# Kernel tuning notes

Hardware: AMD Instinct MI355X
Metric: run time of the kernel (lower is better)

## Reference

```python
import jax, jax.numpy as jnp
import numpy as np

B, N, D = 4, 4096, 512
K = 16384          # codebook size
NUM_Q = 2          # residual quantizers (shared codebook)


def setup_inputs() -> dict:
    key = jax.random.key(0)
    ks = jax.random.split(key, 6)
    s = 1.0 / np.sqrt(D)
    return {
        "x": jax.random.normal(ks[0], (B, N, D), dtype=jnp.float32),
        "enc_w": jax.random.normal(ks[1], (D, D), dtype=jnp.float32) * s,
        "enc_b": jnp.zeros((D,), dtype=jnp.float32),
        "codebook": jax.random.normal(ks[2], (K, D), dtype=jnp.float32),
        "dec_w": jax.random.normal(ks[3], (D, D), dtype=jnp.float32) * s,
        "dec_b": jnp.zeros((D,), dtype=jnp.float32),
    }


def _residual_vq(z, codebook):
    # z: [B, N, D] -> flatten tokens
    flat = z.reshape(-1, z.shape[-1])          # [T, D]
    c_sq = jnp.sum(codebook * codebook, axis=-1)  # [K]
    q_sum = jnp.zeros_like(flat)
    residual = flat
    for _ in range(NUM_Q):
        # argmin of ||r - c||^2 == argmin of (||c||^2 - 2 r.c); skip ||r||^2
        dists = c_sq[None, :] - 2.0 * (residual @ codebook.T)  # [T, K]
        idx = jnp.argmin(dists, axis=-1)                       # [T]
        q = codebook[idx]                                      # gather [T, D]
        q_sum = q_sum + q
        residual = residual - q
    return q_sum.reshape(z.shape)


def reference(x, enc_w, enc_b, codebook, dec_w, dec_b):
    z = x @ enc_w.T + enc_b                     # encoder Linear(512 -> 512)
    q = _residual_vq(z, codebook)               # sum of per-stage code vectors
    z_tilde = z + jax.lax.stop_gradient(q - z)  # straight-through estimator
    x_recon = z_tilde @ dec_w.T + dec_b         # decoder Linear(512 -> 512)
    return x_recon
```

## Files before the change

kernel.cpp:

```cpp
#include <hip/hip_runtime.h>
#include <stdint.h>

constexpr int TT = 16384;
constexpr int DD = 512;
constexpr int KK = 16384;
constexpr int TOPK = 8;

typedef __bf16 bf16x8 __attribute__((ext_vector_type(8)));
typedef __bf16 bf16x4 __attribute__((ext_vector_type(4)));
typedef float f32x4 __attribute__((ext_vector_type(4)));

typedef const __attribute__((address_space(1))) void* gas_ptr;
typedef __attribute__((address_space(3))) void* las_ptr;

__device__ __forceinline__ unsigned long long pack_di(float d, int idx) {
    uint32_t u = __float_as_uint(d);
    u = (u & 0x80000000u) ? ~u : (u | 0x80000000u);
    return ((unsigned long long)u << 32) | (uint32_t)idx;
}

__device__ __forceinline__ unsigned long long umin64(unsigned long long a,
                                                     unsigned long long b) {
    return a < b ? a : b;
}
__device__ __forceinline__ uint32_t umin32(uint32_t a, uint32_t b) { return a < b ? a : b; }
__device__ __forceinline__ uint32_t umax32(uint32_t a, uint32_t b) { return a > b ? a : b; }

__device__ __forceinline__ uint32_t sortable(float d) {
    uint32_t u = __float_as_uint(d);
    return u ^ ((uint32_t)((int32_t)u >> 31) | 0x80000000u);
}

template<int MODE>
__global__ __launch_bounds__(256)
void gemm_mfma(const float* __restrict__ A, const float* __restrict__ A2,
               const float* __restrict__ W, const float* __restrict__ bias,
               float* __restrict__ out0, float* __restrict__ out1,
               __bf16* __restrict__ out2)
{
    __shared__ __bf16 Ah[128 * 64], Al[128 * 64];
    __shared__ __bf16 Bh[128 * 64], Bl[128 * 64];
    const int tid = threadIdx.x;
    const int lane = tid & 63;
    const int w = tid >> 6;
    const int row0 = blockIdx.y * 128;
    const int col0 = blockIdx.x * 128;

    f32x4 acc[2][8] = {};

    const int sr = tid >> 4;
    const int scol = (tid & 15) * 4;
    const int lcol = (((scol >> 3) ^ (sr & 7)) << 3) + (scol & 7);

    int a_off[2], b_off[8];
    #pragma unroll
    for (int mi = 0; mi < 2; ++mi) {
        const int ar = w * 32 + mi * 16 + (lane & 15);
        a_off[mi] = ar * 64 + (((lane >> 4) ^ (ar & 7)) << 3);
    }
    #pragma unroll
    for (int ni = 0; ni < 8; ++ni) {
        const int br = ni * 16 + (lane & 15);
        b_off[ni] = br * 64 + (((lane >> 4) ^ (br & 7)) << 3);
    }

    for (int kb = 0; kb < 512; kb += 64) {
        __syncthreads();
        #pragma unroll
        for (int i = 0; i < 8; ++i) {
            const int r = i * 16 + sr;
            float4 v = *(const float4*)(A + (size_t)(row0 + r) * 512 + kb + scol);
            if (MODE == 1) {
                const float4 u = *(const float4*)(A2 + (size_t)(row0 + r) * 512 + kb + scol);
                v.x -= u.x; v.y -= u.y; v.z -= u.z; v.w -= u.w;
            }
            bf16x4 hv, lv;
            hv[0] = (__bf16)v.x; hv[1] = (__bf16)v.y; hv[2] = (__bf16)v.z; hv[3] = (__bf16)v.w;
            lv[0] = (__bf16)(v.x - (float)hv[0]); lv[1] = (__bf16)(v.y - (float)hv[1]);
            lv[2] = (__bf16)(v.z - (float)hv[2]); lv[3] = (__bf16)(v.w - (float)hv[3]);
            *(bf16x4*)(Ah + r * 64 + lcol) = hv;
            *(bf16x4*)(Al + r * 64 + lcol) = lv;

            const float4 x = *(const float4*)(W + (size_t)(col0 + r) * 512 + kb + scol);
            bf16x4 hw, lw;
            hw[0] = (__bf16)x.x; hw[1] = (__bf16)x.y; hw[2] = (__bf16)x.z; hw[3] = (__bf16)x.w;
            lw[0] = (__bf16)(x.x - (float)hw[0]); lw[1] = (__bf16)(x.y - (float)hw[1]);
            lw[2] = (__bf16)(x.z - (float)hw[2]); lw[3] = (__bf16)(x.w - (float)hw[3]);
            *(bf16x4*)(Bh + r * 64 + lcol) = hw;
            *(bf16x4*)(Bl + r * 64 + lcol) = lw;
        }
        __syncthreads();
        #pragma unroll
        for (int s = 0; s < 2; ++s) {
            const int sx = s * 32;
            bf16x8 ah[2], al[2];
            #pragma unroll
            for (int mi = 0; mi < 2; ++mi) {
                ah[mi] = *(const bf16x8*)(Ah + (a_off[mi] ^ sx));
                al[mi] = *(const bf16x8*)(Al + (a_off[mi] ^ sx));
            }
            #pragma unroll
            for (int ni = 0; ni < 8; ++ni) {
                const bf16x8 bh = *(const bf16x8*)(Bh + (b_off[ni] ^ sx));
                const bf16x8 bl = *(const bf16x8*)(Bl + (b_off[ni] ^ sx));
                #pragma unroll
                for (int mi = 0; mi < 2; ++mi) {
                    acc[mi][ni] = __builtin_amdgcn_mfma_f32_16x16x32_bf16(ah[mi], bh, acc[mi][ni], 0, 0, 0);
                    acc[mi][ni] = __builtin_amdgcn_mfma_f32_16x16x32_bf16(ah[mi], bl, acc[mi][ni], 0, 0, 0);
                    acc[mi][ni] = __builtin_amdgcn_mfma_f32_16x16x32_bf16(al[mi], bh, acc[mi][ni], 0, 0, 0);
                }
            }
        }
    }

    #pragma unroll
    for (int mi = 0; mi < 2; ++mi) {
        #pragma unroll
        for (int reg = 0; reg < 4; ++reg) {
            const int row = row0 + w * 32 + mi * 16 + (lane >> 4) * 4 + reg;
            #pragma unroll
            for (int ni = 0; ni < 8; ++ni) {
                const int col = col0 + ni * 16 + (lane & 15);
                const float o = acc[mi][ni][reg] + bias[col];
                out0[(size_t)row * 512 + col] = o;
                if (MODE == 0) {
                    out1[(size_t)row * 512 + col] = o;
                    out2[(size_t)row * 512 + col] = (__bf16)o;
                }
            }
        }
    }
}

constexpr int CHAIN = 8;
constexpr int NSTEP = 16 * CHAIN;
constexpr size_t TILE_A = 128 * 512;

__global__ __launch_bounds__(256, 3)
void dist_approx4(const __bf16* __restrict__ Rh,
                  const __bf16* __restrict__ Ch,
                  const float* __restrict__ csq,
                  uint32_t* __restrict__ winners)
{
    __shared__ __bf16 As[2][128 * 32];
    __shared__ __bf16 Bs[2][128 * 32];

    const int tid  = threadIdx.x;
    const int lane = tid & 63;
    const int w    = tid >> 6;
    const int wm   = w >> 1;
    const int wn   = w & 1;

    const int b    = blockIdx.x;
    const int xcd  = b & 7;
    const int i    = b >> 3;
    const int ct   = xcd * 16 + (i & 15);
    const int tg   = i >> 4;
    const int col0 = ct << 7;
    const int rowb = tg << 10;

    f32x4 acc[4][4] = {};

    const int s_r = tid >> 2;
    const int s_c = (tid & 3) ^ ((s_r >> 1) & 3);
    const __bf16* aS = Rh + (size_t)(rowb + s_r) * 512 + s_c * 8;
    const __bf16* bS = Ch + (size_t)(col0 + s_r) * 512 + s_c * 8;
    __bf16* const lA0 = &As[0][0]; __bf16* const lA1 = &As[1][0];
    __bf16* const lB0 = &Bs[0][0]; __bf16* const lB1 = &Bs[1][0];

#define AOFF(q) ((size_t)((q) >> 4) * TILE_A + (size_t)((q) & 15) * 32)
#define BOFF(q) ((size_t)((q) & 15) * 32)

#define STAGE(SRC, UOFF, DST)                                                      \
    {                                                                              \
        __builtin_amdgcn_global_load_lds((gas_ptr)((SRC) + (UOFF)),                \
                                         (las_ptr)((DST) + w * 512), 16, 0, 0);    \
        __builtin_amdgcn_global_load_lds((gas_ptr)((SRC) + (UOFF) + 64 * 512),     \
                                         (las_ptr)((DST) + 64 * 32 + w * 512), 16, 0, 0); \
    }

    int aoff[4], boff[4];
    #pragma unroll
    for (int mi = 0; mi < 4; ++mi) {
        const int r = wm * 64 + mi * 16 + (lane & 15);
        aoff[mi] = r * 32 + ((((lane >> 4) ^ ((r >> 1) & 3))) << 3);
    }
    #pragma unroll
    for (int ni = 0; ni < 4; ++ni) {
        const int r = wn * 64 + ni * 16 + (lane & 15);
        boff[ni] = r * 32 + ((((lane >> 4) ^ ((r >> 1) & 3))) << 3);
    }

#define BAR __builtin_amdgcn_s_barrier()
#define LGKM0 { asm volatile("s_waitcnt lgkmcnt(0)" ::: "memory"); \
                __builtin_amdgcn_sched_barrier(0); }
#define MFMA16(AF, BV)                                                         \
    {                                                                          \
        __builtin_amdgcn_s_setprio(1);                                         \
        _Pragma("unroll")                                                      \
        for (int mi = 0; mi < 4; ++mi) {                                       \
            _Pragma("unroll")                                                  \
            for (int ni = 0; ni < 4; ++ni)                                     \
                acc[mi][ni] = __builtin_amdgcn_mfma_f32_16x16x32_bf16(         \
                    (AF)[mi], (BV)[ni], acc[mi][ni], 0, 0, 0);                 \
        }                                                                      \
        __builtin_amdgcn_s_setprio(0);                                         \
    }

#define STEP(LA, LB, S)                                                        \
    {                                                                          \
        _Pragma("unroll")                                                      \
        for (int mi = 0; mi < 4; ++mi) af[mi] = *(const bf16x8*)((LA) + aoff[mi]); \
        _Pragma("unroll")                                                      \
        for (int ni = 0; ni < 4; ++ni) bfr[ni] = *(const bf16x8*)((LB) + boff[ni]); \
        LGKM0;                                                                 \
        BAR;                                                                   \
        const bool more_ = (S) + 2 < NSTEP;                                    \
        if (more_) {                                                           \
            STAGE(aS, AOFF((S) + 2), (LA));                                    \
            STAGE(bS, BOFF((S) + 2), (LB));                                    \
        }                                                                      \
        MFMA16(af, bfr);                                                       \
        if (more_) { asm volatile("s_waitcnt vmcnt(4)" ::: "memory"); }        \
        else       { asm volatile("s_waitcnt vmcnt(0)" ::: "memory"); }        \
        BAR;                                                                   \
    }

    float csv[4];
    #pragma unroll
    for (int ni = 0; ni < 4; ++ni)
        csv[ni] = csq[col0 + wn * 64 + ni * 16 + (lane & 15)];
    const int gt = (col0 >> 6) + wn;

    STAGE(aS, AOFF(0), lA0);
    STAGE(bS, BOFF(0), lB0);
    STAGE(aS, AOFF(1), lA1);
    STAGE(bS, BOFF(1), lB1);
    asm volatile("s_waitcnt vmcnt(4)" ::: "memory");
    BAR;

    bf16x8 af[4], bfr[4];

    for (int it = 0; it < 8 * CHAIN; ++it) {
        STEP(lA0, lB0, 2 * it);
        STEP(lA1, lB1, 2 * it + 1);

        if ((it & 7) == 7) {
            const int r0t = rowb + (it >> 3) * 128;
            #pragma unroll
            for (int mi = 0; mi < 4; ++mi) {
                #pragma unroll
                for (int reg = 0; reg < 4; ++reg) {
                    uint32_t bk = 0xFFFFFFFFu, sk = 0xFFFFFFFFu;
                    #pragma unroll
                    for (int ni = 0; ni < 4; ++ni) {
                        const float d = fmaf(-2.0f, acc[mi][ni][reg], csv[ni]);
                        const uint32_t key = (sortable(d) & 0xFFFFFFC0u)
                                           | (uint32_t)(ni * 16 + (lane & 15));
                        const uint32_t nb = umin32(bk, key);
                        sk = umin32(sk, umax32(bk, key));
                        bk = nb;
                    }
                    #pragma unroll
                    for (int m = 1; m < 16; m <<= 1) {
                        const uint32_t ob = __shfl_xor((int)bk, m, 16);
                        const uint32_t os = __shfl_xor((int)sk, m, 16);
                        const uint32_t nb = umin32(bk, ob);
                        sk = umin32(umin32(sk, os), umax32(bk, ob));
                        bk = nb;
                    }
                    if ((lane & 15) == 0) {
                        const int row = r0t + wm * 64 + mi * 16 + (lane >> 4) * 4 + reg;
                        uint2 v; v.x = bk; v.y = sk;
                        *(uint2*)(winners + (size_t)row * 512 + gt * 2) = v;
                    }
                }
            }
            #pragma unroll
            for (int mi = 0; mi < 4; ++mi)
                #pragma unroll
                for (int ni = 0; ni < 4; ++ni)
                    acc[mi][ni] = (f32x4){0.f, 0.f, 0.f, 0.f};
        }
    }
#undef STEP
#undef STAGE
#undef AOFF
#undef BOFF
#undef BAR
#undef LGKM0
#undef MFMA16
}

__global__ __launch_bounds__(256)
void select_rescore(const uint32_t* __restrict__ winners,
                    const float* __restrict__ CB, const float* __restrict__ csq,
                    float* __restrict__ R, __bf16* __restrict__ R16)
{
    const int w = threadIdx.x >> 6;
    const int lane = threadIdx.x & 63;
    const int token = blockIdx.x * 4 + w;

    const uint32_t* wt = winners + (size_t)token * 512;
    uint4 q0 = *(const uint4*)(wt + lane * 8);
    uint4 q1 = *(const uint4*)(wt + lane * 8 + 4);
    uint32_t k32[8] = {q0.x, q0.y, q0.z, q0.w, q1.x, q1.y, q1.z, q1.w};

    unsigned long long v[8];
    #pragma unroll
    for (int j = 0; j < 8; ++j) {
        const int gcol = ((lane * 8 + j) >> 1) * 64 + (int)(k32[j] & 63u);
        v[j] = ((unsigned long long)k32[j] << 32) | (uint32_t)gcol;
    }

    unsigned long long cand[TOPK];
    #pragma unroll
    for (int t = 0; t < TOPK; ++t) {
        unsigned long long mm = v[0];
        #pragma unroll
        for (int j = 1; j < 8; ++j) mm = umin64(mm, v[j]);
        #pragma unroll
        for (int m = 1; m < 64; m <<= 1)
            mm = umin64(mm, __shfl_xor(mm, m, 64));
        cand[t] = mm;
        #pragma unroll
        for (int j = 0; j < 8; ++j) if (v[j] == mm) v[j] = ~0ull;
    }

    float4 r0 = *(const float4*)(R + (size_t)token * 512 + lane * 8);
    float4 r1 = *(const float4*)(R + (size_t)token * 512 + lane * 8 + 4);

    unsigned long long best = ~0ull;
    #pragma unroll
    for (int t = 0; t < TOPK; ++t) {
        const int col = (int)(cand[t] & 0xFFFFFFFFull);
        const float4 c0 = *(const float4*)(CB + (size_t)col * 512 + lane * 8);
        const float4 c1 = *(const float4*)(CB + (size_t)col * 512 + lane * 8 + 4);
        float dot = r0.x * c0.x;
        dot = fmaf(r0.y, c0.y, dot); dot = fmaf(r0.z, c0.z, dot);
        dot = fmaf(r0.w, c0.w, dot); dot = fmaf(r1.x, c1.x, dot);
        dot = fmaf(r1.y, c1.y, dot); dot = fmaf(r1.z, c1.z, dot);
        dot = fmaf(r1.w, c1.w, dot);
        #pragma unroll
        for (int m = 1; m < 64; m <<= 1) dot += __shfl_xor(dot, m, 64);
        const float d = fmaf(-2.0f, dot, csq[col]);
        best = umin64(best, pack_di(d, col));
    }

    const int bcol = (int)(best & 0xFFFFFFFFull);
    const float4 c0 = *(const float4*)(CB + (size_t)bcol * 512 + lane * 8);
    const float4 c1 = *(const float4*)(CB + (size_t)bcol * 512 + lane * 8 + 4);
    r0.x -= c0.x; r0.y -= c0.y; r0.z -= c0.z; r0.w -= c0.w;
    r1.x -= c1.x; r1.y -= c1.y; r1.z -= c1.z; r1.w -= c1.w;
    *(float4*)(R + (size_t)token * 512 + lane * 8) = r0;
    *(float4*)(R + (size_t)token * 512 + lane * 8 + 4) = r1;
    bf16x8 h;
    h[0] = (__bf16)r0.x; h[1] = (__bf16)r0.y; h[2] = (__bf16)r0.z; h[3] = (__bf16)r0.w;
    h[4] = (__bf16)r1.x; h[5] = (__bf16)r1.y; h[6] = (__bf16)r1.z; h[7] = (__bf16)r1.w;
    *(bf16x8*)(R16 + (size_t)token * 512 + lane * 8) = h;
}

__global__ __launch_bounds__(256)
void prep_cb(const float* __restrict__ CB, float* __restrict__ c_sq,
             __bf16* __restrict__ cb16)
{
    const int wave = threadIdx.x >> 6;
    const int lane = threadIdx.x & 63;
    const int row = blockIdx.x * 4 + wave;
    const float* p = CB + (size_t)row * DD + lane * 8;
    const float4 a = *(const float4*)p;
    const float4 b = *(const float4*)(p + 4);
    bf16x8 h;
    h[0] = (__bf16)a.x; h[1] = (__bf16)a.y; h[2] = (__bf16)a.z; h[3] = (__bf16)a.w;
    h[4] = (__bf16)b.x; h[5] = (__bf16)b.y; h[6] = (__bf16)b.z; h[7] = (__bf16)b.w;
    *(bf16x8*)(cb16 + (size_t)row * DD + lane * 8) = h;
    float s = a.x*a.x + a.y*a.y + a.z*a.z + a.w*a.w
            + b.x*b.x + b.y*b.y + b.z*b.z + b.w*b.w;
    #pragma unroll
    for (int m = 1; m < 64; m <<= 1) s += __shfl_xor(s, m, 64);
    if (lane == 0) c_sq[row] = s;
}

extern "C" void kernel_launch(void* const* d_in, const int* in_sizes, int n_in,
                              void* d_out, int out_size, void* d_ws, size_t ws_size,
                              hipStream_t stream)
{
    const float* x    = (const float*)d_in[0];
    const float* encw = (const float*)d_in[1];
    const float* encb = (const float*)d_in[2];
    const float* cb   = (const float*)d_in[3];
    const float* decw = (const float*)d_in[4];
    const float* decb = (const float*)d_in[5];
    float* out = (float*)d_out;

    float* z    = (float*)d_ws;
    float* r    = z + (size_t)TT * DD;
    __bf16* cb16 = (__bf16*)(r + (size_t)TT * DD);
    __bf16* r16  = cb16 + (size_t)KK * DD;
    float* csq  = (float*)(r16 + (size_t)TT * DD);
    uint32_t* winners = (uint32_t*)d_out;

    const dim3 blk(256);

    gemm_mfma<0><<<dim3(DD / 128, TT / 128), blk, 0, stream>>>(
        x, nullptr, encw, encb, z, r, r16);

    prep_cb<<<dim3(KK / 4), blk, 0, stream>>>(cb, csq, cb16);

    for (int s = 0; s < 2; ++s) {
        dist_approx4<<<dim3((KK / 128) * (TT / 128 / CHAIN)), dim3(256), 0, stream>>>(
            r16, cb16, csq, winners);
        select_rescore<<<dim3(TT / 4), blk, 0, stream>>>(winners, cb, csq, r, r16);
    }

    gemm_mfma<1><<<dim3(DD / 128, TT / 128), blk, 0, stream>>>(
        z, r, decw, decb, out, nullptr, nullptr);
}
```

Baseline: 1.036 ms.

## Load distance-GEMM A operand directly into registers instead of via LDS

The residual (A) tile of the distance GEMM is no longer staged through shared memory with global_load_lds. Each wave now loads its A fragments straight from global memory into registers, prefetched one k-step ahead with a pair of register buffers, while the codebook (B) tile stays double-buffered in LDS. This cuts LDS traffic and shared-memory footprint for A. The cost is that the two waves sharing the same rows each fetch them from global/cache, using uncoalesced 16-byte per-lane accesses, and the waitcnt now has to cover the A prefetch latency within one MFMA block.

After: 1.488 ms. 1.44x slower.

```diff
diff --git a/kernel.cpp b/kernel.cpp
--- a/kernel.cpp
+++ b/kernel.cpp
@@ -142,7 +142,6 @@
                   const float* __restrict__ csq,
                   uint32_t* __restrict__ winners)
 {
-    __shared__ __bf16 As[2][128 * 32];
     __shared__ __bf16 Bs[2][128 * 32];
 
     const int tid  = threadIdx.x;
@@ -163,28 +162,24 @@
 
     const int s_r = tid >> 2;
     const int s_c = (tid & 3) ^ ((s_r >> 1) & 3);
-    const __bf16* aS = Rh + (size_t)(rowb + s_r) * 512 + s_c * 8;
     const __bf16* bS = Ch + (size_t)(col0 + s_r) * 512 + s_c * 8;
-    __bf16* const lA0 = &As[0][0]; __bf16* const lA1 = &As[1][0];
     __bf16* const lB0 = &Bs[0][0]; __bf16* const lB1 = &Bs[1][0];
+
+    const __bf16* aF = Rh + (size_t)(rowb + wm * 64 + (lane & 15)) * 512
+                          + (lane >> 4) * 8;
 
 #define AOFF(q) ((size_t)((q) >> 4) * TILE_A + (size_t)((q) & 15) * 32)
 #define BOFF(q) ((size_t)((q) & 15) * 32)
 
-#define STAGE(SRC, UOFF, DST)                                                      \
+#define STAGEB(UOFF, DST)                                                          \
     {                                                                              \
-        __builtin_amdgcn_global_load_lds((gas_ptr)((SRC) + (UOFF)),                \
+        __builtin_amdgcn_global_load_lds((gas_ptr)(bS + (UOFF)),                   \
                                          (las_ptr)((DST) + w * 512), 16, 0, 0);    \
-        __builtin_amdgcn_global_load_lds((gas_ptr)((SRC) + (UOFF) + 64 * 512),     \
+        __builtin_amdgcn_global_load_lds((gas_ptr)(bS + (UOFF) + 64 * 512),        \
                                          (las_ptr)((DST) + 64 * 32 + w * 512), 16, 0, 0); \
     }
 
-    int aoff[4], boff[4];
-    #pragma unroll
-    for (int mi = 0; mi < 4; ++mi) {
-        const int r = wm * 64 + mi * 16 + (lane & 15);
-        aoff[mi] = r * 32 + ((((lane >> 4) ^ ((r >> 1) & 3))) << 3);
-    }
+    int boff[4];
     #pragma unroll
     for (int ni = 0; ni < 4; ++ni) {
         const int r = wn * 64 + ni * 16 + (lane & 15);
@@ -207,22 +202,23 @@
         __builtin_amdgcn_s_setprio(0);                                         \
     }
 
-#define STEP(LA, LB, S)                                                        \
+#define STEP(LB, AFC, AFN, S)                                                  \
     {                                                                          \
-        _Pragma("unroll")                                                      \
-        for (int mi = 0; mi < 4; ++mi) af[mi] = *(const bf16x8*)((LA) + aoff[mi]); \
+        if ((S) + 1 < NSTEP) {                                                 \
+            _Pragma("unroll")                                                  \
+            for (int mi = 0; mi < 4; ++mi)                                     \
+                (AFN)[mi] = *(const bf16x8*)(aF + (size_t)mi * (16 * 512)      \
+                                              + AOFF((S) + 1));                \
+            __builtin_amdgcn_sched_barrier(0);         \
+        }                                                                      \
         _Pragma("unroll")                                                      \
         for (int ni = 0; ni < 4; ++ni) bfr[ni] = *(const bf16x8*)((LB) + boff[ni]); \
         LGKM0;                                                                 \
         BAR;                                                                   \
-        const bool more_ = (S) + 2 < NSTEP;                                    \
-        if (more_) {                                                           \
-            STAGE(aS, AOFF((S) + 2), (LA));                                    \
-            STAGE(bS, BOFF((S) + 2), (LB));                                    \
-        }                                                                      \
-        MFMA16(af, bfr);                                                       \
-        if (more_) { asm volatile("s_waitcnt vmcnt(4)" ::: "memory"); }        \
-        else       { asm volatile("s_waitcnt vmcnt(0)" ::: "memory"); }        \
+        if ((S) + 2 < NSTEP) STAGEB(BOFF((S) + 2), (LB));                      \
+        MFMA16(AFC, bfr);                                                      \
+        if ((S) + 2 < NSTEP) { asm volatile("s_waitcnt vmcnt(2)" ::: "memory"); } \
+        else                 { asm volatile("s_waitcnt vmcnt(0)" ::: "memory"); } \
         BAR;                                                                   \
     }
 
@@ -232,18 +228,19 @@
         csv[ni] = csq[col0 + wn * 64 + ni * 16 + (lane & 15)];
     const int gt = (col0 >> 6) + wn;
 
-    STAGE(aS, AOFF(0), lA0);
-    STAGE(bS, BOFF(0), lB0);
-    STAGE(aS, AOFF(1), lA1);
-    STAGE(bS, BOFF(1), lB1);
-    asm volatile("s_waitcnt vmcnt(4)" ::: "memory");
+    bf16x8 afA[4], afB[4], bfr[4];
+
+    STAGEB(BOFF(0), lB0);
+    STAGEB(BOFF(1), lB1);
+    #pragma unroll
+    for (int mi = 0; mi < 4; ++mi)
+        afA[mi] = *(const bf16x8*)(aF + (size_t)mi * (16 * 512) + AOFF(0));
+    asm volatile("s_waitcnt vmcnt(0)" ::: "memory");
     BAR;
 
-    bf16x8 af[4], bfr[4];
-
     for (int it = 0; it < 8 * CHAIN; ++it) {
-        STEP(lA0, lB0, 2 * it);
-        STEP(lA1, lB1, 2 * it + 1);
+        STEP(lB0, afA, afB, 2 * it);
+        STEP(lB1, afB, afA, 2 * it + 1);
 
         if ((it & 7) == 7) {
             const int r0t = rowb + (it >> 3) * 128;
@@ -284,7 +281,7 @@
         }
     }
 #undef STEP
-#undef STAGE
+#undef STAGEB
 #undef AOFF
 #undef BOFF
 #undef BAR
```
